# Kernel tuning notes

Measured on AMD Instinct MI355X. Metric: run time of the kernel, lower is better.

Reference implementation:

```python
import jax, jax.numpy as jnp
import numpy as np

B, S, E = 8, 2048, 1024
DROPOUT_P = 0.1


def setup_inputs() -> dict:
    key = jax.random.key(0)
    kq, kk, kv, km, kw, kb = jax.random.split(key, 6)
    query = jax.random.normal(kq, (B, S, E), dtype=jnp.float32)
    key_t = jax.random.normal(kk, (B, S, E), dtype=jnp.float32)
    value = jax.random.normal(kv, (B, S, E), dtype=jnp.float32)
    # inverted dropout mask: keep with prob 1-p, scale kept by 1/(1-p)
    keep = jax.random.bernoulli(km, 1.0 - DROPOUT_P, (B, S, S))
    dropout_mask = keep.astype(jnp.float32) / (1.0 - DROPOUT_P)
    Wout = jax.random.normal(kw, (E, E), dtype=jnp.float32) * (E ** -0.5)
    bout = jax.random.normal(kb, (E,), dtype=jnp.float32) * 0.01
    return {
        "query": query,
        "key": key_t,
        "value": value,
        "dropout_mask": dropout_mask,
        "Wout": Wout,
        "bout": bout,
        "inv_scale_factor": 32,  # sqrt(E) = sqrt(1024)
    }


def reference(query, key, value, dropout_mask, Wout, bout, inv_scale_factor):
    # scores: [B, S, S]
    scores = jnp.einsum("bqd,bkd->bqk", query, key) / jnp.float32(inv_scale_factor)
    probs = jax.nn.softmax(scores, axis=-1)
    probs = probs * dropout_mask  # inverted dropout
    attn = jnp.einsum("bqk,bkd->bqd", probs, value)  # [B, S, E]
    # fc_out: torch Linear -> x @ W.T + b
    return jnp.einsum("bqd,ed->bqe", attn, Wout) + bout
```

## Files before the change

### kernel.cpp

```cpp
#include <hip/hip_runtime.h>
#include <cstdint>
#include <cstddef>

typedef short short8 __attribute__((ext_vector_type(8)));
typedef float f32x4 __attribute__((ext_vector_type(4)));

static __device__ __forceinline__ ushort f2bf(float f) {
  union { float f; uint32_t u; } v; v.f = f;
  uint32_t u = v.u + 0x7fffu + ((v.u >> 16) & 1u);
  return (ushort)(u >> 16);
}
static __device__ __forceinline__ float b2f(uint32_t u) {
  union { uint32_t u; float f; } v; v.u = u << 16;
  return v.f;
}

static __device__ __forceinline__ void g2lds16(const ushort* g, ushort* lds) {
  __builtin_amdgcn_global_load_lds(
      (const __attribute__((address_space(1))) void*)(uintptr_t)g,
      (__attribute__((address_space(3))) void*)(uintptr_t)lds,
      16, 0, 0);
}

__global__ __launch_bounds__(256) void convert_f32_bf16(
    const float* __restrict__ src, ushort* __restrict__ dst) {
  const size_t i = ((size_t)blockIdx.x * 256 + threadIdx.x) * 8;
  const float4 a = *(const float4*)(src + i);
  const float4 b = *(const float4*)(src + i + 4);
  ushort4 o0, o1;
  o0.x = f2bf(a.x); o0.y = f2bf(a.y); o0.z = f2bf(a.z); o0.w = f2bf(a.w);
  o1.x = f2bf(b.x); o1.y = f2bf(b.y); o1.z = f2bf(b.z); o1.w = f2bf(b.w);
  *(ushort4*)(dst + i) = o0;
  *(ushort4*)(dst + i + 4) = o1;
}

__global__ __launch_bounds__(256) void transpose_convert_v(
    const float* __restrict__ V, ushort* __restrict__ Vt) {
  __shared__ float t[32][33];
  const int b = blockIdx.z;
  const int d0 = blockIdx.x * 32;
  const int k0 = blockIdx.y * 32;
  const int tx = threadIdx.x, ty = threadIdx.y;
  const float* Vb = V + (size_t)b * 2048 * 1024;
  ushort* Vtb = Vt + (size_t)b * 1024 * 2048;
#pragma unroll
  for (int j = 0; j < 32; j += 8)
    t[ty + j][tx] = Vb[(size_t)(k0 + ty + j) * 1024 + d0 + tx];
  __syncthreads();
#pragma unroll
  for (int j = 0; j < 32; j += 8)
    Vtb[(size_t)(d0 + ty + j) * 2048 + k0 + tx] = f2bf(t[tx][ty + j]);
}

template <bool B_F32, bool OUT_BF16, bool BIAS>
__global__ __launch_bounds__(256) void gemm_bt(
    const ushort* __restrict__ Ap, const void* __restrict__ Bp,
    void* __restrict__ Cp, int M, int N, int K,
    size_t sA, size_t sB, size_t sC, float scale,
    const float* __restrict__ bias) {
  constexpr int BK = 64;
  constexpr int LDB = B_F32 ? 72 : 64;
  __shared__ __align__(16) ushort As[128 * 64];
  __shared__ __align__(16) ushort Bs[128 * LDB];
  const int tid = threadIdx.x;
  const int z = blockIdx.z;
  const int bm = blockIdx.y, bn = blockIdx.x;
  const int lane = tid & 63, w = tid >> 6;
  const int quad = lane >> 4, l16 = lane & 15;
  const int row0 = (w & 1) * 64, col0 = (w >> 1) * 64;
  const int srow = lane >> 3;
  const int scol = (lane & 7) * 8;

  f32x4 acc[4][4];
#pragma unroll
  for (int i = 0; i < 4; ++i)
#pragma unroll
    for (int j = 0; j < 4; ++j) acc[i][j] = (f32x4){0.f, 0.f, 0.f, 0.f};

  const ushort* Abase = Ap + sA * z + (size_t)bm * 128 * K;

  for (int k0 = 0; k0 < K; k0 += BK) {
#pragma unroll
    for (int i = 0; i < 4; ++i) {
      const int rbase = w * 8 + i * 32;
      g2lds16(Abase + (size_t)(rbase + srow) * K + k0 + scol, &As[rbase * 64]);
    }
    if constexpr (B_F32) {
      const float* B = (const float*)Bp + sB * z + (size_t)bn * 128 * K + k0;
      int r = tid >> 4;
      const int c = (tid & 15) * 4;
#pragma unroll
      for (int i = 0; i < 8; ++i, r += 16) {
        const float4 v = *(const float4*)(B + (size_t)r * K + c);
        ushort4 o;
        o.x = f2bf(v.x); o.y = f2bf(v.y); o.z = f2bf(v.z); o.w = f2bf(v.w);
        *(ushort4*)&Bs[r * LDB + c] = o;
      }
    } else {
      const ushort* B = (const ushort*)Bp + sB * z + (size_t)bn * 128 * K + k0;
#pragma unroll
      for (int i = 0; i < 4; ++i) {
        const int rbase = w * 8 + i * 32;
        g2lds16(B + (size_t)(rbase + srow) * K + scol, &Bs[rbase * 64]);
      }
    }
    __syncthreads();
#pragma unroll
    for (int kc = 0; kc < BK; kc += 32) {
      short8 af[4], bfr[4];
#pragma unroll
      for (int tm = 0; tm < 4; ++tm)
        af[tm] = *(const short8*)&As[(row0 + tm * 16 + l16) * 64 + kc + quad * 8];
#pragma unroll
      for (int tn = 0; tn < 4; ++tn)
        bfr[tn] = *(const short8*)&Bs[(col0 + tn * 16 + l16) * LDB + kc + quad * 8];
#pragma unroll
      for (int tm = 0; tm < 4; ++tm)
#pragma unroll
        for (int tn = 0; tn < 4; ++tn)
          acc[tm][tn] = __builtin_amdgcn_mfma_f32_16x16x32_bf16(
              af[tm], bfr[tn], acc[tm][tn], 0, 0, 0);
    }
    __syncthreads();
  }
#pragma unroll
  for (int tn = 0; tn < 4; ++tn) {
    const int gc = bn * 128 + col0 + tn * 16 + l16;
    const float bv = BIAS ? bias[gc] : 0.f;
#pragma unroll
    for (int tm = 0; tm < 4; ++tm) {
      const int grb = bm * 128 + row0 + tm * 16 + quad * 4;
#pragma unroll
      for (int r = 0; r < 4; ++r) {
        const float v = acc[tm][tn][r] * scale + bv;
        const size_t idx = (size_t)(grb + r) * N + gc;
        if constexpr (OUT_BF16)
          ((ushort*)Cp + sC * z)[idx] = f2bf(v);
        else
          ((float*)Cp + sC * z)[idx] = v;
      }
    }
  }
}

__global__ __launch_bounds__(256) void softmax_dropout(
    ushort* __restrict__ P, const float* __restrict__ mask) {
  const int row = blockIdx.x;
  const size_t off = (size_t)row * 2048 + (size_t)threadIdx.x * 8;
  ushort* p = P + off;
  const float* mk = mask + off;
  const uint4 raw = *(const uint4*)p;
  float s[8];
  s[0] = b2f(raw.x & 0xffffu); s[1] = b2f(raw.x >> 16);
  s[2] = b2f(raw.y & 0xffffu); s[3] = b2f(raw.y >> 16);
  s[4] = b2f(raw.z & 0xffffu); s[5] = b2f(raw.z >> 16);
  s[6] = b2f(raw.w & 0xffffu); s[7] = b2f(raw.w >> 16);
  float m = s[0];
#pragma unroll
  for (int i = 1; i < 8; ++i) m = fmaxf(m, s[i]);
#pragma unroll
  for (int o = 32; o >= 1; o >>= 1) m = fmaxf(m, __shfl_xor(m, o));
  __shared__ float redm[4], reds[4];
  const int wv = threadIdx.x >> 6;
  if ((threadIdx.x & 63) == 0) redm[wv] = m;
  __syncthreads();
  m = fmaxf(fmaxf(redm[0], redm[1]), fmaxf(redm[2], redm[3]));
  float e[8], l = 0.f;
#pragma unroll
  for (int i = 0; i < 8; ++i) { e[i] = __expf(s[i] - m); l += e[i]; }
#pragma unroll
  for (int o = 32; o >= 1; o >>= 1) l += __shfl_xor(l, o);
  if ((threadIdx.x & 63) == 0) reds[wv] = l;
  __syncthreads();
  l = (reds[0] + reds[1]) + (reds[2] + reds[3]);
  const float inv = 1.0f / l;
  const float4 m0 = *(const float4*)mk;
  const float4 m1 = *(const float4*)(mk + 4);
  float q[8];
  q[0] = e[0] * inv * m0.x; q[1] = e[1] * inv * m0.y;
  q[2] = e[2] * inv * m0.z; q[3] = e[3] * inv * m0.w;
  q[4] = e[4] * inv * m1.x; q[5] = e[5] * inv * m1.y;
  q[6] = e[6] * inv * m1.z; q[7] = e[7] * inv * m1.w;
  uint4 o;
  o.x = (uint32_t)f2bf(q[0]) | ((uint32_t)f2bf(q[1]) << 16);
  o.y = (uint32_t)f2bf(q[2]) | ((uint32_t)f2bf(q[3]) << 16);
  o.z = (uint32_t)f2bf(q[4]) | ((uint32_t)f2bf(q[5]) << 16);
  o.w = (uint32_t)f2bf(q[6]) | ((uint32_t)f2bf(q[7]) << 16);
  *(uint4*)p = o;
}

extern "C" void kernel_launch(void* const* d_in, const int* in_sizes, int n_in,
                              void* d_out, int out_size, void* d_ws,
                              size_t ws_size, hipStream_t stream) {
  (void)in_sizes; (void)n_in; (void)out_size; (void)ws_size;
  const float* Q    = (const float*)d_in[0];
  const float* Kmat = (const float*)d_in[1];
  const float* V    = (const float*)d_in[2];
  const float* mask = (const float*)d_in[3];
  const float* W    = (const float*)d_in[4];
  const float* bout = (const float*)d_in[5];
  float* out = (float*)d_out;

  ushort* RegA = (ushort*)d_ws;
  ushort* RegB = RegA + (size_t)16 * 1024 * 1024;
  ushort* P    = RegB + (size_t)16 * 1024 * 1024;

  convert_f32_bf16<<<dim3(8192), 256, 0, stream>>>(Q, RegA);
  convert_f32_bf16<<<dim3(8192), 256, 0, stream>>>(Kmat, RegB);
  gemm_bt<false, true, false><<<dim3(16, 16, 8), 256, 0, stream>>>(
      RegA, RegB, P, 2048, 2048, 1024,
      (size_t)2048 * 1024, (size_t)2048 * 1024, (size_t)2048 * 2048,
      1.0f / 32.0f, nullptr);
  transpose_convert_v<<<dim3(32, 64, 8), dim3(32, 8), 0, stream>>>(V, RegA);
  softmax_dropout<<<dim3(16384), 256, 0, stream>>>(P, mask);
  gemm_bt<false, true, false><<<dim3(8, 16, 8), 256, 0, stream>>>(
      P, RegA, RegB, 2048, 1024, 2048,
      (size_t)2048 * 2048, (size_t)1024 * 2048, (size_t)2048 * 1024,
      1.0f, nullptr);
  gemm_bt<true, false, true><<<dim3(8, 128, 1), 256, 0, stream>>>(
      RegB, W, out, 16384, 1024, 1024, 0, 0, 0, 1.0f, bout);
}
```

Before: 625.7 us.

## XOR-swizzle GEMM LDS tiles, merge Q/K conversion, widen V transpose stores

Applies an XOR swizzle to the 16-byte column groups written by global_load_lds into the bf16 A and B LDS tiles. The MFMA fragment reads use the same swizzle so they no longer hit the same LDS banks across rows of the 64-wide tile. Separately, the Q and K fp32-to-bf16 conversions are merged into one launch, and the V transpose now packs two bf16 values per 32-bit store. The fp32-B path keeps its padded, unswizzled layout for B.

```diff
diff --git a/kernel.cpp b/kernel.cpp
--- a/kernel.cpp
+++ b/kernel.cpp
@@ -22,9 +22,13 @@
       16, 0, 0);
 }
 
-__global__ __launch_bounds__(256) void convert_f32_bf16(
-    const float* __restrict__ src, ushort* __restrict__ dst) {
-  const size_t i = ((size_t)blockIdx.x * 256 + threadIdx.x) * 8;
+__global__ __launch_bounds__(256) void convert_qk_bf16(
+    const float* __restrict__ Q, const float* __restrict__ K,
+    ushort* __restrict__ Qb, ushort* __restrict__ Kb) {
+  const bool second = blockIdx.x >= 8192;
+  const float* src = second ? K : Q;
+  ushort* dst = second ? Kb : Qb;
+  const size_t i = ((size_t)(blockIdx.x & 8191) * 256 + threadIdx.x) * 8;
   const float4 a = *(const float4*)(src + i);
   const float4 b = *(const float4*)(src + i + 4);
   ushort4 o0, o1;
@@ -47,9 +51,16 @@
   for (int j = 0; j < 32; j += 8)
     t[ty + j][tx] = Vb[(size_t)(k0 + ty + j) * 1024 + d0 + tx];
   __syncthreads();
-#pragma unroll
-  for (int j = 0; j < 32; j += 8)
-    Vtb[(size_t)(d0 + ty + j) * 2048 + k0 + tx] = f2bf(t[tx][ty + j]);
+  const int l = ty * 32 + tx;
+  const int kk = (l & 15) * 2;
+  const int dd = l >> 4;
+#pragma unroll
+  for (int p = 0; p < 2; ++p) {
+    const int d = dd + p * 16;
+    const uint32_t val =
+        (uint32_t)f2bf(t[kk][d]) | ((uint32_t)f2bf(t[kk + 1][d]) << 16);
+    *(uint32_t*)&Vtb[(size_t)(d0 + d) * 2048 + k0 + kk] = val;
+  }
 }
 
 template <bool B_F32, bool OUT_BF16, bool BIAS>
@@ -69,7 +80,7 @@
   const int quad = lane >> 4, l16 = lane & 15;
   const int row0 = (w & 1) * 64, col0 = (w >> 1) * 64;
   const int srow = lane >> 3;
-  const int scol = (lane & 7) * 8;
+  const int scol = ((lane & 7) ^ srow) * 8;
 
   f32x4 acc[4][4];
 #pragma unroll
@@ -107,13 +118,21 @@
     __syncthreads();
 #pragma unroll
     for (int kc = 0; kc < BK; kc += 32) {
+      const int gidx = (kc >> 3) + quad;
       short8 af[4], bfr[4];
 #pragma unroll
-      for (int tm = 0; tm < 4; ++tm)
-        af[tm] = *(const short8*)&As[(row0 + tm * 16 + l16) * 64 + kc + quad * 8];
-#pragma unroll
-      for (int tn = 0; tn < 4; ++tn)
-        bfr[tn] = *(const short8*)&Bs[(col0 + tn * 16 + l16) * LDB + kc + quad * 8];
+      for (int tm = 0; tm < 4; ++tm) {
+        const int row = row0 + tm * 16 + l16;
+        af[tm] = *(const short8*)&As[row * 64 + ((gidx ^ (row & 7)) << 3)];
+      }
+#pragma unroll
+      for (int tn = 0; tn < 4; ++tn) {
+        const int row = col0 + tn * 16 + l16;
+        if constexpr (B_F32)
+          bfr[tn] = *(const short8*)&Bs[row * LDB + kc + quad * 8];
+        else
+          bfr[tn] = *(const short8*)&Bs[row * 64 + ((gidx ^ (row & 7)) << 3)];
+      }
 #pragma unroll
       for (int tm = 0; tm < 4; ++tm)
 #pragma unroll
@@ -205,8 +224,7 @@
   ushort* RegB = RegA + (size_t)16 * 1024 * 1024;
   ushort* P    = RegB + (size_t)16 * 1024 * 1024;
 
-  convert_f32_bf16<<<dim3(8192), 256, 0, stream>>>(Q, RegA);
-  convert_f32_bf16<<<dim3(8192), 256, 0, stream>>>(Kmat, RegB);
+  convert_qk_bf16<<<dim3(16384), 256, 0, stream>>>(Q, Kmat, RegA, RegB);
   gemm_bt<false, true, false><<<dim3(16, 16, 8), 256, 0, stream>>>(
       RegA, RegB, P, 2048, 2048, 1024,
       (size_t)2048 * 1024, (size_t)2048 * 1024, (size_t)2048 * 2048,
```

Result: faster. 600.0 us (-4.1%).
